# Performance work log

Measured on AMD Instinct MI355X. Metric: run time of the kernel, lower is better.

## Reference

```python
import jax, jax.numpy as jnp
import numpy as np

D_MODEL = 512
NUM_HEADS = 8
D_K = D_MODEL // NUM_HEADS


def setup_inputs() -> dict:
    key = jax.random.key(0)
    ks = jax.random.split(key, 11)
    B, S = 2, 4096
    std = max(0.02, min((1.0 / D_MODEL) ** 0.5, 0.5))
    xavier = (6.0 / (D_MODEL + D_MODEL)) ** 0.5
    return {
        "Q": jax.random.normal(ks[0], (B, S, D_MODEL), jnp.float32),
        "K": jax.random.normal(ks[1], (B, S, D_MODEL), jnp.float32),
        "V": jax.random.normal(ks[2], (B, S, D_MODEL), jnp.float32),
        # torch Linear convention: weight [out, in], y = x @ W.T + b
        "Wq": std * jax.random.truncated_normal(ks[3], -2.0, 2.0, (D_MODEL, D_MODEL), jnp.float32),
        "bq": jnp.zeros((D_MODEL,), jnp.float32),
        "Wk": std * jax.random.truncated_normal(ks[4], -2.0, 2.0, (D_MODEL, D_MODEL), jnp.float32),
        "bk": jnp.zeros((D_MODEL,), jnp.float32),
        "Wv": std * jax.random.truncated_normal(ks[5], -2.0, 2.0, (D_MODEL, D_MODEL), jnp.float32),
        "bv": jnp.zeros((D_MODEL,), jnp.float32),
        "Wo": jax.random.uniform(ks[6], (D_MODEL, D_MODEL), jnp.float32, -xavier, xavier),
        "bo": jnp.zeros((D_MODEL,), jnp.float32),
    }


def _split_heads(x):
    B, S, _ = x.shape
    return x.reshape(B, S, NUM_HEADS, D_K).transpose(0, 2, 1, 3)  # [B,H,S,dk]


def reference(Q, K, V, Wq, bq, Wk, bk, Wv, bv, Wo, bo):
    B, S, _ = Q.shape
    q = _split_heads(Q @ Wq.T + bq)
    k = _split_heads(K @ Wk.T + bk)
    v = _split_heads(V @ Wv.T + bv)
    scores = jnp.einsum("bhqd,bhkd->bhqk", q, k) / (D_K ** 0.5)  # [B,H,S,S]
    causal = jnp.tril(jnp.ones((S, S), bool))  # mask=True path
    scores = jnp.where(causal[None, None], scores, jnp.float32(-1e9))
    attn = jax.nn.softmax(scores, axis=-1)
    out = jnp.einsum("bhqk,bhkd->bhqd", attn, v)
    out = out.transpose(0, 2, 1, 3).reshape(B, S, D_MODEL)
    return out @ Wo.T + bo, attn
```

## Files before the change

kernel.cpp:

```cpp
#include <hip/hip_runtime.h>
#include <stdint.h>

#define B_  2
#define H_  8
#define S_  4096
#define DM_ 512
#define DK_ 64
#define BH_ (B_*H_)

using f32x4 = __attribute__((ext_vector_type(4))) float;
using s16x8 = __attribute__((ext_vector_type(8))) short;
using u16x4 = __attribute__((ext_vector_type(4))) unsigned short;

__device__ __forceinline__ unsigned short f2bf(float f) {
    unsigned int u = __float_as_uint(f);
    u += 0x7FFFu + ((u >> 16) & 1u);
    return (unsigned short)(u >> 16);
}
__device__ __forceinline__ float bf2f(unsigned short h) {
    return __uint_as_float(((unsigned int)h) << 16);
}

template<int MODE>
__global__ __launch_bounds__(256) void proj_kernel(
        const float* __restrict__ X, const float* __restrict__ W,
        const float* __restrict__ bias, unsigned short* __restrict__ Y,
        float scale)
{
    __shared__ __align__(16) unsigned short xh[64*40], xl[64*40];
    __shared__ __align__(16) unsigned short wh[64*40], wl[64*40];
    const int tid  = threadIdx.x;
    const int wave = tid >> 6, lane = tid & 63, lq = lane >> 4, lr = lane & 15;
    const int m0 = blockIdx.x * 64, n0 = blockIdx.y * 64;

    f32x4 acc[4] = {{0.f,0.f,0.f,0.f},{0.f,0.f,0.f,0.f},
                    {0.f,0.f,0.f,0.f},{0.f,0.f,0.f,0.f}};

    for (int kk = 0; kk < 16; ++kk) {
        __syncthreads();
#pragma unroll
        for (int p = 0; p < 2; ++p) {
            int idx = tid + p*256;
            int row = idx >> 3, seg = idx & 7;
            float4 xv = *(const float4*)&X[(size_t)(m0+row)*DM_ + kk*32 + seg*4];
            float4 wv = *(const float4*)&W[(size_t)(n0+row)*DM_ + kk*32 + seg*4];
            float xs4[4] = {xv.x, xv.y, xv.z, xv.w};
            float ws4[4] = {wv.x, wv.y, wv.z, wv.w};
            u16x4 xhi, xlo, whi, wlo;
#pragma unroll
            for (int i = 0; i < 4; ++i) {
                unsigned short h = f2bf(xs4[i]); xhi[i] = h; xlo[i] = f2bf(xs4[i] - bf2f(h));
                unsigned short g = f2bf(ws4[i]); whi[i] = g; wlo[i] = f2bf(ws4[i] - bf2f(g));
            }
            *(u16x4*)&xh[row*40 + seg*4] = xhi;
            *(u16x4*)&xl[row*40 + seg*4] = xlo;
            *(u16x4*)&wh[row*40 + seg*4] = whi;
            *(u16x4*)&wl[row*40 + seg*4] = wlo;
        }
        __syncthreads();
        const int ar = wave*16 + lr;
        s16x8 ah = *(const s16x8*)&xh[ar*40 + lq*8];
        s16x8 al = *(const s16x8*)&xl[ar*40 + lq*8];
#pragma unroll
        for (int nt = 0; nt < 4; ++nt) {
            int br = nt*16 + lr;
            s16x8 bh8 = *(const s16x8*)&wh[br*40 + lq*8];
            s16x8 bl8 = *(const s16x8*)&wl[br*40 + lq*8];
            acc[nt] = __builtin_amdgcn_mfma_f32_16x16x32_bf16(ah, bh8, acc[nt], 0, 0, 0);
            acc[nt] = __builtin_amdgcn_mfma_f32_16x16x32_bf16(ah, bl8, acc[nt], 0, 0, 0);
            acc[nt] = __builtin_amdgcn_mfma_f32_16x16x32_bf16(al, bh8, acc[nt], 0, 0, 0);
        }
    }
#pragma unroll
    for (int nt = 0; nt < 4; ++nt)
#pragma unroll
        for (int r = 0; r < 4; ++r) {
            int m = m0 + wave*16 + lq*4 + r;
            int n = n0 + nt*16 + lr;
            float v = (acc[nt][r] + bias[n]) * scale;
            int b = m >> 12, s = m & 4095;
            int h = n >> 6,  d = n & 63;
            size_t addr;
            if (MODE == 0) addr = ((size_t)((b*H_ + h)*S_ + s))*DK_ + d;
            else           addr = ((size_t)((b*H_ + h)*DK_ + d))*S_ + s;
            Y[addr] = f2bf(v);
        }
}

__global__ __launch_bounds__(256) void stats_kernel(
        const unsigned short* __restrict__ qb, const unsigned short* __restrict__ kb,
        float* __restrict__ lsum)
{
    __shared__ __align__(16) unsigned short qs[64*72], ks[32*72];
    const int tid  = threadIdx.x;
    const int wave = tid >> 6, lane = tid & 63, lq = lane >> 4, lr = lane & 15;
    const int bh = blockIdx.y;
    const int s0 = blockIdx.x * 64;

#pragma unroll
    for (int p = 0; p < 2; ++p) {
        int idx = tid + p*256;
        int row = idx >> 3, seg = idx & 7;
        *(s16x8*)&qs[row*72 + seg*8] =
            *(const s16x8*)&qb[((size_t)bh*S_ + s0 + row)*DK_ + seg*8];
    }
    __syncthreads();
    const int ar = wave*16 + lr;
    s16x8 aq0 = *(const s16x8*)&qs[ar*72 +  0 + lq*8];
    s16x8 aq1 = *(const s16x8*)&qs[ar*72 + 32 + lq*8];

    float lacc[4] = {0.f, 0.f, 0.f, 0.f};
    const int jtmax = (s0 + 63) >> 5;
    for (int jt = 0; jt <= jtmax; ++jt) {
        __syncthreads();
        {
            int row = tid >> 3, seg = tid & 7;
            *(s16x8*)&ks[row*72 + seg*8] =
                *(const s16x8*)&kb[((size_t)bh*S_ + jt*32 + row)*DK_ + seg*8];
        }
        __syncthreads();
#pragma unroll
        for (int nt = 0; nt < 2; ++nt) {
            int br = nt*16 + lr;
            s16x8 b0 = *(const s16x8*)&ks[br*72 +  0 + lq*8];
            s16x8 b1 = *(const s16x8*)&ks[br*72 + 32 + lq*8];
            f32x4 sc = {0.f,0.f,0.f,0.f};
            sc = __builtin_amdgcn_mfma_f32_16x16x32_bf16(aq0, b0, sc, 0, 0, 0);
            sc = __builtin_amdgcn_mfma_f32_16x16x32_bf16(aq1, b1, sc, 0, 0, 0);
            int j = jt*32 + nt*16 + lr;
#pragma unroll
            for (int r = 0; r < 4; ++r) {
                int sq = s0 + wave*16 + lq*4 + r;
                lacc[r] += (j <= sq) ? __expf(sc[r] - 16.f) : 0.f;
            }
        }
    }
#pragma unroll
    for (int r = 0; r < 4; ++r) {
        float v = lacc[r];
        for (int off = 1; off < 16; off <<= 1) v += __shfl_xor(v, off, 64);
        if (lr == 0) lsum[(size_t)bh*S_ + s0 + wave*16 + lq*4 + r] = v;
    }
}

__global__ __launch_bounds__(256) void attn_kernel(
        const unsigned short* __restrict__ qb, const unsigned short* __restrict__ kb,
        const unsigned short* __restrict__ vtb, const float* __restrict__ lsum,
        float* __restrict__ attn, unsigned short* __restrict__ oacc)
{
    __shared__ __align__(16) unsigned short qs[64*72], ks[32*72], vs[64*40];
    __shared__ __align__(16) unsigned short ps[4][16*40];
    __shared__ float invl[64];
    const int tid  = threadIdx.x;
    const int wave = tid >> 6, lane = tid & 63, lq = lane >> 4, lr = lane & 15;
    const int bh = blockIdx.y;
    const int s0 = blockIdx.x * 64;

#pragma unroll
    for (int p = 0; p < 2; ++p) {
        int idx = tid + p*256;
        int row = idx >> 3, seg = idx & 7;
        *(s16x8*)&qs[row*72 + seg*8] =
            *(const s16x8*)&qb[((size_t)bh*S_ + s0 + row)*DK_ + seg*8];
    }
    if (tid < 64) invl[tid] = 1.0f / lsum[(size_t)bh*S_ + s0 + tid];
    __syncthreads();
    const int ar = wave*16 + lr;
    s16x8 aq0 = *(const s16x8*)&qs[ar*72 +  0 + lq*8];
    s16x8 aq1 = *(const s16x8*)&qs[ar*72 + 32 + lq*8];
    float il[4];
#pragma unroll
    for (int r = 0; r < 4; ++r) il[r] = invl[wave*16 + lq*4 + r];

    f32x4 O[4] = {{0.f,0.f,0.f,0.f},{0.f,0.f,0.f,0.f},
                  {0.f,0.f,0.f,0.f},{0.f,0.f,0.f,0.f}};
    const int jtcomp = (s0 + 63) >> 5;

    for (int jt = 0; jt < S_/32; ++jt) {
        if (jt <= jtcomp) {
            __syncthreads();
            {
                int row = tid >> 3, seg = tid & 7;
                *(s16x8*)&ks[row*72 + seg*8] =
                    *(const s16x8*)&kb[((size_t)bh*S_ + jt*32 + row)*DK_ + seg*8];
            }
            {
                int d = tid >> 2, seg = tid & 3;
                *(s16x8*)&vs[d*40 + seg*8] =
                    *(const s16x8*)&vtb[((size_t)bh*DK_ + d)*S_ + jt*32 + seg*8];
            }
            __syncthreads();
#pragma unroll
            for (int nt = 0; nt < 2; ++nt) {
                int br = nt*16 + lr;
                s16x8 b0 = *(const s16x8*)&ks[br*72 +  0 + lq*8];
                s16x8 b1 = *(const s16x8*)&ks[br*72 + 32 + lq*8];
                f32x4 sc = {0.f,0.f,0.f,0.f};
                sc = __builtin_amdgcn_mfma_f32_16x16x32_bf16(aq0, b0, sc, 0, 0, 0);
                sc = __builtin_amdgcn_mfma_f32_16x16x32_bf16(aq1, b1, sc, 0, 0, 0);
                int j = jt*32 + nt*16 + lr;
#pragma unroll
                for (int r = 0; r < 4; ++r) {
                    int sq = s0 + wave*16 + lq*4 + r;
                    float p = (j <= sq) ? __expf(sc[r] - 16.f) : 0.f;
                    float a = p * il[r];
                    attn[((size_t)bh*S_ + sq)*S_ + j] = a;
                    ps[wave][(lq*4 + r)*40 + nt*16 + lr] = f2bf(a);
                }
            }
            __syncthreads();
            s16x8 ap = *(const s16x8*)&ps[wave][lr*40 + lq*8];
#pragma unroll
            for (int nt = 0; nt < 4; ++nt) {
                s16x8 bv = *(const s16x8*)&vs[(nt*16 + lr)*40 + lq*8];
                O[nt] = __builtin_amdgcn_mfma_f32_16x16x32_bf16(ap, bv, O[nt], 0, 0, 0);
            }
        } else {
#pragma unroll
            for (int p = 0; p < 2; ++p) {
                int idx = tid + p*256;
                int row = idx >> 3, c4 = idx & 7;
                float4 z = {0.f, 0.f, 0.f, 0.f};
                *(float4*)&attn[((size_t)bh*S_ + s0 + row)*S_ + jt*32 + c4*4] = z;
            }
        }
    }
    const int b = bh >> 3, h = bh & 7;
#pragma unroll
    for (int nt = 0; nt < 4; ++nt)
#pragma unroll
        for (int r = 0; r < 4; ++r) {
            int s = s0 + wave*16 + lq*4 + r;
            oacc[((size_t)(b*S_ + s))*DM_ + h*DK_ + nt*16 + lr] = f2bf(O[nt][r]);
        }
}

__global__ __launch_bounds__(256) void outproj_kernel(
        const unsigned short* __restrict__ Xin, const float* __restrict__ W,
        const float* __restrict__ bias, float* __restrict__ out)
{
    __shared__ __align__(16) unsigned short xs[64*40], wh[64*40];
    const int tid  = threadIdx.x;
    const int wave = tid >> 6, lane = tid & 63, lq = lane >> 4, lr = lane & 15;
    const int m0 = blockIdx.x * 64, n0 = blockIdx.y * 64;

    f32x4 acc[4] = {{0.f,0.f,0.f,0.f},{0.f,0.f,0.f,0.f},
                    {0.f,0.f,0.f,0.f},{0.f,0.f,0.f,0.f}};

    for (int kk = 0; kk < 16; ++kk) {
        __syncthreads();
        {
            int row = tid >> 2, seg = tid & 3;
            *(s16x8*)&xs[row*40 + seg*8] =
                *(const s16x8*)&Xin[(size_t)(m0+row)*DM_ + kk*32 + seg*8];
        }
#pragma unroll
        for (int p = 0; p < 2; ++p) {
            int idx = tid + p*256;
            int row = idx >> 3, seg = idx & 7;
            float4 wv = *(const float4*)&W[(size_t)(n0+row)*DM_ + kk*32 + seg*4];
            u16x4 whi;
            whi[0] = f2bf(wv.x); whi[1] = f2bf(wv.y);
            whi[2] = f2bf(wv.z); whi[3] = f2bf(wv.w);
            *(u16x4*)&wh[row*40 + seg*4] = whi;
        }
        __syncthreads();
        s16x8 a = *(const s16x8*)&xs[(wave*16 + lr)*40 + lq*8];
#pragma unroll
        for (int nt = 0; nt < 4; ++nt) {
            s16x8 b = *(const s16x8*)&wh[(nt*16 + lr)*40 + lq*8];
            acc[nt] = __builtin_amdgcn_mfma_f32_16x16x32_bf16(a, b, acc[nt], 0, 0, 0);
        }
    }
#pragma unroll
    for (int nt = 0; nt < 4; ++nt)
#pragma unroll
        for (int r = 0; r < 4; ++r) {
            int m = m0 + wave*16 + lq*4 + r;
            int n = n0 + nt*16 + lr;
            out[(size_t)m*DM_ + n] = acc[nt][r] + bias[n];
        }
}

extern "C" void kernel_launch(void* const* d_in, const int* in_sizes, int n_in,
                              void* d_out, int out_size, void* d_ws, size_t ws_size,
                              hipStream_t stream)
{
    const float* Q  = (const float*)d_in[0];
    const float* K  = (const float*)d_in[1];
    const float* V  = (const float*)d_in[2];
    const float* Wq = (const float*)d_in[3];  const float* bq = (const float*)d_in[4];
    const float* Wk = (const float*)d_in[5];  const float* bk = (const float*)d_in[6];
    const float* Wv = (const float*)d_in[7];  const float* bv = (const float*)d_in[8];
    const float* Wo = (const float*)d_in[9];  const float* bo = (const float*)d_in[10];

    char* ws = (char*)d_ws;
    const size_t QKV_BYTES = (size_t)BH_ * S_ * DK_ * sizeof(unsigned short);
    unsigned short* qbf  = (unsigned short*)(ws);
    unsigned short* kbf  = (unsigned short*)(ws + QKV_BYTES);
    unsigned short* vtb  = (unsigned short*)(ws + 2*QKV_BYTES);
    float*          lsum = (float*)(ws + 3*QKV_BYTES);
    unsigned short* oacc = (unsigned short*)(ws + 3*QKV_BYTES + (size_t)BH_*S_*sizeof(float));

    float* out0 = (float*)d_out;
    float* attn = out0 + (size_t)B_ * S_ * DM_;

    dim3 blk(256);
    proj_kernel<0><<<dim3(128, 8), blk, 0, stream>>>(Q, Wq, bq, qbf, 0.125f);
    proj_kernel<0><<<dim3(128, 8), blk, 0, stream>>>(K, Wk, bk, kbf, 1.0f);
    proj_kernel<1><<<dim3(128, 8), blk, 0, stream>>>(V, Wv, bv, vtb, 1.0f);
    stats_kernel  <<<dim3(64, 16), blk, 0, stream>>>(qbf, kbf, lsum);
    attn_kernel   <<<dim3(64, 16), blk, 0, stream>>>(qbf, kbf, vtb, lsum, attn, oacc);
    outproj_kernel<<<dim3(128, 8), blk, 0, stream>>>(oacc, Wo, bo, out0);
}
```

Baseline: 1.497 ms.

## Pre-split inputs to bf16 hi/lo, widen K tiles to 64 across kernels

Adds separate conversion kernels that split the inputs and weights into bf16 hi/lo arrays once, so the projection GEMMs no longer redo the split for every output tile. The GEMMs, stats and attention kernels now use 64-wide K/key tiles, which halves loop iterations and barriers. The attention kernel also replaces a block barrier with a per-wave LDS wait and groups the attention-matrix stores after the PV MFMAs. The cost is extra launches and extra global traffic for the converted copies, plus larger shared-memory use.

```diff
diff --git a/kernel.cpp b/kernel.cpp
--- a/kernel.cpp
+++ b/kernel.cpp
@@ -11,6 +11,7 @@
 using f32x4 = __attribute__((ext_vector_type(4))) float;
 using s16x8 = __attribute__((ext_vector_type(8))) short;
 using u16x4 = __attribute__((ext_vector_type(4))) unsigned short;
+using u16x8 = __attribute__((ext_vector_type(8))) unsigned short;
 
 __device__ __forceinline__ unsigned short f2bf(float f) {
     unsigned int u = __float_as_uint(f);
@@ -21,14 +22,42 @@
     return __uint_as_float(((unsigned int)h) << 16);
 }
 
+__global__ __launch_bounds__(256) void convert_split(const float* __restrict__ in,
+        unsigned short* __restrict__ hi, unsigned short* __restrict__ lo, int n4)
+{
+    for (int i = blockIdx.x*256 + threadIdx.x; i < n4; i += gridDim.x*256) {
+        float4 v = ((const float4*)in)[i];
+        float s4[4] = {v.x, v.y, v.z, v.w};
+        u16x4 h, l;
+#pragma unroll
+        for (int j = 0; j < 4; ++j) {
+            unsigned short hh = f2bf(s4[j]);
+            h[j] = hh; l[j] = f2bf(s4[j] - bf2f(hh));
+        }
+        ((u16x4*)hi)[i] = h;
+        ((u16x4*)lo)[i] = l;
+    }
+}
+
+__global__ __launch_bounds__(256) void convert_hi(const float* __restrict__ in,
+        unsigned short* __restrict__ hi, int n4)
+{
+    for (int i = blockIdx.x*256 + threadIdx.x; i < n4; i += gridDim.x*256) {
+        float4 v = ((const float4*)in)[i];
+        u16x4 h;
+        h[0] = f2bf(v.x); h[1] = f2bf(v.y); h[2] = f2bf(v.z); h[3] = f2bf(v.w);
+        ((u16x4*)hi)[i] = h;
+    }
+}
+
 template<int MODE>
 __global__ __launch_bounds__(256) void proj_kernel(
-        const float* __restrict__ X, const float* __restrict__ W,
-        const float* __restrict__ bias, unsigned short* __restrict__ Y,
-        float scale)
-{
-    __shared__ __align__(16) unsigned short xh[64*40], xl[64*40];
-    __shared__ __align__(16) unsigned short wh[64*40], wl[64*40];
+        const unsigned short* __restrict__ Xh, const unsigned short* __restrict__ Xl,
+        const unsigned short* __restrict__ Wh, const unsigned short* __restrict__ Wl,
+        const float* __restrict__ bias, unsigned short* __restrict__ Y, float scale)
+{
+    __shared__ __align__(16) unsigned short xh[64*72], xl[64*72];
+    __shared__ __align__(16) unsigned short wh[64*72], wl[64*72];
     const int tid  = threadIdx.x;
     const int wave = tid >> 6, lane = tid & 63, lq = lane >> 4, lr = lane & 15;
     const int m0 = blockIdx.x * 64, n0 = blockIdx.y * 64;
@@ -36,39 +65,38 @@
     f32x4 acc[4] = {{0.f,0.f,0.f,0.f},{0.f,0.f,0.f,0.f},
                     {0.f,0.f,0.f,0.f},{0.f,0.f,0.f,0.f}};
 
-    for (int kk = 0; kk < 16; ++kk) {
+    for (int kk = 0; kk < 8; ++kk) {
         __syncthreads();
 #pragma unroll
         for (int p = 0; p < 2; ++p) {
             int idx = tid + p*256;
             int row = idx >> 3, seg = idx & 7;
-            float4 xv = *(const float4*)&X[(size_t)(m0+row)*DM_ + kk*32 + seg*4];
-            float4 wv = *(const float4*)&W[(size_t)(n0+row)*DM_ + kk*32 + seg*4];
-            float xs4[4] = {xv.x, xv.y, xv.z, xv.w};
-            float ws4[4] = {wv.x, wv.y, wv.z, wv.w};
-            u16x4 xhi, xlo, whi, wlo;
-#pragma unroll
-            for (int i = 0; i < 4; ++i) {
-                unsigned short h = f2bf(xs4[i]); xhi[i] = h; xlo[i] = f2bf(xs4[i] - bf2f(h));
-                unsigned short g = f2bf(ws4[i]); whi[i] = g; wlo[i] = f2bf(ws4[i] - bf2f(g));
-            }
-            *(u16x4*)&xh[row*40 + seg*4] = xhi;
-            *(u16x4*)&xl[row*40 + seg*4] = xlo;
-            *(u16x4*)&wh[row*40 + seg*4] = whi;
-            *(u16x4*)&wl[row*40 + seg*4] = wlo;
+            size_t xoff = (size_t)(m0+row)*DM_ + kk*64 + seg*8;
+            size_t woff = (size_t)(n0+row)*DM_ + kk*64 + seg*8;
+            *(u16x8*)&xh[row*72 + seg*8] = *(const u16x8*)&Xh[xoff];
+            *(u16x8*)&xl[row*72 + seg*8] = *(const u16x8*)&Xl[xoff];
+            *(u16x8*)&wh[row*72 + seg*8] = *(const u16x8*)&Wh[woff];
+            *(u16x8*)&wl[row*72 + seg*8] = *(const u16x8*)&Wl[woff];
         }
         __syncthreads();
         const int ar = wave*16 + lr;
-        s16x8 ah = *(const s16x8*)&xh[ar*40 + lq*8];
-        s16x8 al = *(const s16x8*)&xl[ar*40 + lq*8];
+        s16x8 ah0 = *(const s16x8*)&xh[ar*72 +  0 + lq*8];
+        s16x8 ah1 = *(const s16x8*)&xh[ar*72 + 32 + lq*8];
+        s16x8 al0 = *(const s16x8*)&xl[ar*72 +  0 + lq*8];
+        s16x8 al1 = *(const s16x8*)&xl[ar*72 + 32 + lq*8];
 #pragma unroll
         for (int nt = 0; nt < 4; ++nt) {
             int br = nt*16 + lr;
-            s16x8 bh8 = *(const s16x8*)&wh[br*40 + lq*8];
-            s16x8 bl8 = *(const s16x8*)&wl[br*40 + lq*8];
-            acc[nt] = __builtin_amdgcn_mfma_f32_16x16x32_bf16(ah, bh8, acc[nt], 0, 0, 0);
-            acc[nt] = __builtin_amdgcn_mfma_f32_16x16x32_bf16(ah, bl8, acc[nt], 0, 0, 0);
-            acc[nt] = __builtin_amdgcn_mfma_f32_16x16x32_bf16(al, bh8, acc[nt], 0, 0, 0);
+            s16x8 bh0 = *(const s16x8*)&wh[br*72 +  0 + lq*8];
+            s16x8 bh1 = *(const s16x8*)&wh[br*72 + 32 + lq*8];
+            s16x8 bl0 = *(const s16x8*)&wl[br*72 +  0 + lq*8];
+            s16x8 bl1 = *(const s16x8*)&wl[br*72 + 32 + lq*8];
+            acc[nt] = __builtin_amdgcn_mfma_f32_16x16x32_bf16(ah0, bh0, acc[nt], 0, 0, 0);
+            acc[nt] = __builtin_amdgcn_mfma_f32_16x16x32_bf16(ah0, bl0, acc[nt], 0, 0, 0);
+            acc[nt] = __builtin_amdgcn_mfma_f32_16x16x32_bf16(al0, bh0, acc[nt], 0, 0, 0);
+            acc[nt] = __builtin_amdgcn_mfma_f32_16x16x32_bf16(ah1, bh1, acc[nt], 0, 0, 0);
+            acc[nt] = __builtin_amdgcn_mfma_f32_16x16x32_bf16(ah1, bl1, acc[nt], 0, 0, 0);
+            acc[nt] = __builtin_amdgcn_mfma_f32_16x16x32_bf16(al1, bh1, acc[nt], 0, 0, 0);
         }
     }
 #pragma unroll
@@ -91,7 +119,7 @@
         const unsigned short* __restrict__ qb, const unsigned short* __restrict__ kb,
         float* __restrict__ lsum)
 {
-    __shared__ __align__(16) unsigned short qs[64*72], ks[32*72];
+    __shared__ __align__(16) unsigned short qs[64*72], ks[64*72];
     const int tid  = threadIdx.x;
     const int wave = tid >> 6, lane = tid & 63, lq = lane >> 4, lr = lane & 15;
     const int bh = blockIdx.y;
@@ -110,24 +138,26 @@
     s16x8 aq1 = *(const s16x8*)&qs[ar*72 + 32 + lq*8];
 
     float lacc[4] = {0.f, 0.f, 0.f, 0.f};
-    const int jtmax = (s0 + 63) >> 5;
+    const int jtmax = blockIdx.x;
     for (int jt = 0; jt <= jtmax; ++jt) {
         __syncthreads();
-        {
-            int row = tid >> 3, seg = tid & 7;
+#pragma unroll
+        for (int p = 0; p < 2; ++p) {
+            int idx = tid + p*256;
+            int row = idx >> 3, seg = idx & 7;
             *(s16x8*)&ks[row*72 + seg*8] =
-                *(const s16x8*)&kb[((size_t)bh*S_ + jt*32 + row)*DK_ + seg*8];
-        }
-        __syncthreads();
-#pragma unroll
-        for (int nt = 0; nt < 2; ++nt) {
+                *(const s16x8*)&kb[((size_t)bh*S_ + jt*64 + row)*DK_ + seg*8];
+        }
+        __syncthreads();
+#pragma unroll
+        for (int nt = 0; nt < 4; ++nt) {
             int br = nt*16 + lr;
             s16x8 b0 = *(const s16x8*)&ks[br*72 +  0 + lq*8];
             s16x8 b1 = *(const s16x8*)&ks[br*72 + 32 + lq*8];
             f32x4 sc = {0.f,0.f,0.f,0.f};
             sc = __builtin_amdgcn_mfma_f32_16x16x32_bf16(aq0, b0, sc, 0, 0, 0);
             sc = __builtin_amdgcn_mfma_f32_16x16x32_bf16(aq1, b1, sc, 0, 0, 0);
-            int j = jt*32 + nt*16 + lr;
+            int j = jt*64 + nt*16 + lr;
 #pragma unroll
             for (int r = 0; r < 4; ++r) {
                 int sq = s0 + wave*16 + lq*4 + r;
@@ -148,8 +178,8 @@
         const unsigned short* __restrict__ vtb, const float* __restrict__ lsum,
         float* __restrict__ attn, unsigned short* __restrict__ oacc)
 {
-    __shared__ __align__(16) unsigned short qs[64*72], ks[32*72], vs[64*40];
-    __shared__ __align__(16) unsigned short ps[4][16*40];
+    __shared__ __align__(16) unsigned short qs[64*72], ks[64*72], vs[64*72];
+    __shared__ __align__(16) unsigned short ps[4][16*72];
     __shared__ float invl[64];
     const int tid  = threadIdx.x;
     const int wave = tid >> 6, lane = tid & 63, lq = lane >> 4, lr = lane & 15;
@@ -174,54 +204,65 @@
 
     f32x4 O[4] = {{0.f,0.f,0.f,0.f},{0.f,0.f,0.f,0.f},
                   {0.f,0.f,0.f,0.f},{0.f,0.f,0.f,0.f}};
-    const int jtcomp = (s0 + 63) >> 5;
-
-    for (int jt = 0; jt < S_/32; ++jt) {
+    const int jtcomp = blockIdx.x;
+
+    for (int jt = 0; jt < S_/64; ++jt) {
         if (jt <= jtcomp) {
             __syncthreads();
-            {
-                int row = tid >> 3, seg = tid & 7;
+#pragma unroll
+            for (int p = 0; p < 2; ++p) {
+                int idx = tid + p*256;
+                int row = idx >> 3, seg = idx & 7;
                 *(s16x8*)&ks[row*72 + seg*8] =
-                    *(const s16x8*)&kb[((size_t)bh*S_ + jt*32 + row)*DK_ + seg*8];
-            }
-            {
-                int d = tid >> 2, seg = tid & 3;
-                *(s16x8*)&vs[d*40 + seg*8] =
-                    *(const s16x8*)&vtb[((size_t)bh*DK_ + d)*S_ + jt*32 + seg*8];
+                    *(const s16x8*)&kb[((size_t)bh*S_ + jt*64 + row)*DK_ + seg*8];
+                *(s16x8*)&vs[row*72 + seg*8] =
+                    *(const s16x8*)&vtb[((size_t)bh*DK_ + row)*S_ + jt*64 + seg*8];
             }
             __syncthreads();
-#pragma unroll
-            for (int nt = 0; nt < 2; ++nt) {
+            float a_all[4][4];
+#pragma unroll
+            for (int nt = 0; nt < 4; ++nt) {
                 int br = nt*16 + lr;
                 s16x8 b0 = *(const s16x8*)&ks[br*72 +  0 + lq*8];
                 s16x8 b1 = *(const s16x8*)&ks[br*72 + 32 + lq*8];
                 f32x4 sc = {0.f,0.f,0.f,0.f};
                 sc = __builtin_amdgcn_mfma_f32_16x16x32_bf16(aq0, b0, sc, 0, 0, 0);
                 sc = __builtin_amdgcn_mfma_f32_16x16x32_bf16(aq1, b1, sc, 0, 0, 0);
-                int j = jt*32 + nt*16 + lr;
+                int j = jt*64 + nt*16 + lr;
 #pragma unroll
                 for (int r = 0; r < 4; ++r) {
                     int sq = s0 + wave*16 + lq*4 + r;
                     float p = (j <= sq) ? __expf(sc[r] - 16.f) : 0.f;
                     float a = p * il[r];
-                    attn[((size_t)bh*S_ + sq)*S_ + j] = a;
-                    ps[wave][(lq*4 + r)*40 + nt*16 + lr] = f2bf(a);
+                    a_all[nt][r] = a;
+                    ps[wave][(lq*4 + r)*72 + nt*16 + lr] = f2bf(a);
                 }
             }
-            __syncthreads();
-            s16x8 ap = *(const s16x8*)&ps[wave][lr*40 + lq*8];
+            asm volatile("s_waitcnt lgkmcnt(0)" ::: "memory");
+            __builtin_amdgcn_sched_barrier(0);
+            s16x8 ap0 = *(const s16x8*)&ps[wave][lr*72 +  0 + lq*8];
+            s16x8 ap1 = *(const s16x8*)&ps[wave][lr*72 + 32 + lq*8];
 #pragma unroll
             for (int nt = 0; nt < 4; ++nt) {
-                s16x8 bv = *(const s16x8*)&vs[(nt*16 + lr)*40 + lq*8];
-                O[nt] = __builtin_amdgcn_mfma_f32_16x16x32_bf16(ap, bv, O[nt], 0, 0, 0);
-            }
+                s16x8 bv0 = *(const s16x8*)&vs[(nt*16 + lr)*72 +  0 + lq*8];
+                s16x8 bv1 = *(const s16x8*)&vs[(nt*16 + lr)*72 + 32 + lq*8];
+                O[nt] = __builtin_amdgcn_mfma_f32_16x16x32_bf16(ap0, bv0, O[nt], 0, 0, 0);
+                O[nt] = __builtin_amdgcn_mfma_f32_16x16x32_bf16(ap1, bv1, O[nt], 0, 0, 0);
+            }
+#pragma unroll
+            for (int nt = 0; nt < 4; ++nt)
+#pragma unroll
+                for (int r = 0; r < 4; ++r) {
+                    int sq = s0 + wave*16 + lq*4 + r;
+                    attn[((size_t)bh*S_ + sq)*S_ + jt*64 + nt*16 + lr] = a_all[nt][r];
+                }
         } else {
 #pragma unroll
-            for (int p = 0; p < 2; ++p) {
+            for (int p = 0; p < 4; ++p) {
                 int idx = tid + p*256;
-                int row = idx >> 3, c4 = idx & 7;
+                int row = idx >> 4, c4 = idx & 15;
                 float4 z = {0.f, 0.f, 0.f, 0.f};
-                *(float4*)&attn[((size_t)bh*S_ + s0 + row)*S_ + jt*32 + c4*4] = z;
+                *(float4*)&attn[((size_t)bh*S_ + s0 + row)*S_ + jt*64 + c4*4] = z;
             }
         }
     }
@@ -236,10 +277,10 @@
 }
 
 __global__ __launch_bounds__(256) void outproj_kernel(
-        const unsigned short* __restrict__ Xin, const float* __restrict__ W,
+        const unsigned short* __restrict__ Xin, const unsigned short* __restrict__ Woh,
         const float* __restrict__ bias, float* __restrict__ out)
 {
-    __shared__ __align__(16) unsigned short xs[64*40], wh[64*40];
+    __shared__ __align__(16) unsigned short xs[64*72], wsm[64*72];
     const int tid  = threadIdx.x;
     const int wave = tid >> 6, lane = tid & 63, lq = lane >> 4, lr = lane & 15;
     const int m0 = blockIdx.x * 64, n0 = blockIdx.y * 64;
@@ -247,29 +288,28 @@
     f32x4 acc[4] = {{0.f,0.f,0.f,0.f},{0.f,0.f,0.f,0.f},
                     {0.f,0.f,0.f,0.f},{0.f,0.f,0.f,0.f}};
 
-    for (int kk = 0; kk < 16; ++kk) {
-        __syncthreads();
-        {
-            int row = tid >> 2, seg = tid & 3;
-            *(s16x8*)&xs[row*40 + seg*8] =
-                *(const s16x8*)&Xin[(size_t)(m0+row)*DM_ + kk*32 + seg*8];
-        }
+    for (int kk = 0; kk < 8; ++kk) {
+        __syncthreads();
 #pragma unroll
         for (int p = 0; p < 2; ++p) {
             int idx = tid + p*256;
             int row = idx >> 3, seg = idx & 7;
-            float4 wv = *(const float4*)&W[(size_t)(n0+row)*DM_ + kk*32 + seg*4];
-            u16x4 whi;
-            whi[0] = f2bf(wv.x); whi[1] = f2bf(wv.y);
-            whi[2] = f2bf(wv.z); whi[3] = f2bf(wv.w);
-            *(u16x4*)&wh[row*40 + seg*4] = whi;
-        }
-        __syncthreads();
-        s16x8 a = *(const s16x8*)&xs[(wave*16 + lr)*40 + lq*8];
+            *(s16x8*)&xs [row*72 + seg*8] =
+                *(const s16x8*)&Xin[(size_t)(m0+row)*DM_ + kk*64 + seg*8];
+            *(s16x8*)&wsm[row*72 + seg*8] =
+                *(const s16x8*)&Woh[(size_t)(n0+row)*DM_ + kk*64 + seg*8];
+        }
+        __syncthreads();
+        const int ar = wave*16 + lr;
+        s16x8 a0 = *(const s16x8*)&xs[ar*72 +  0 + lq*8];
+        s16x8 a1 = *(const s16x8*)&xs[ar*72 + 32 + lq*8];
 #pragma unroll
         for (int nt = 0; nt < 4; ++nt) {
-            s16x8 b = *(const s16x8*)&wh[(nt*16 + lr)*40 + lq*8];
-            acc[nt] = __builtin_amdgcn_mfma_f32_16x16x32_bf16(a, b, acc[nt], 0, 0, 0);
+            int br = nt*16 + lr;
+            s16x8 b0 = *(const s16x8*)&wsm[br*72 +  0 + lq*8];
+            s16x8 b1 = *(const s16x8*)&wsm[br*72 + 32 + lq*8];
+            acc[nt] = __builtin_amdgcn_mfma_f32_16x16x32_bf16(a0, b0, acc[nt], 0, 0, 0);
+            acc[nt] = __builtin_amdgcn_mfma_f32_16x16x32_bf16(a1, b1, acc[nt], 0, 0, 0);
         }
     }
 #pragma unroll
@@ -296,20 +336,44 @@
 
     char* ws = (char*)d_ws;
     const size_t QKV_BYTES = (size_t)BH_ * S_ * DK_ * sizeof(unsigned short);
+    const size_t W_BYTES   = (size_t)DM_ * DM_ * sizeof(unsigned short);
     unsigned short* qbf  = (unsigned short*)(ws);
     unsigned short* kbf  = (unsigned short*)(ws + QKV_BYTES);
     unsigned short* vtb  = (unsigned short*)(ws + 2*QKV_BYTES);
     float*          lsum = (float*)(ws + 3*QKV_BYTES);
     unsigned short* oacc = (unsigned short*)(ws + 3*QKV_BYTES + (size_t)BH_*S_*sizeof(float));
+    char* p = ws + 4*QKV_BYTES + (size_t)BH_*S_*sizeof(float);
+    unsigned short* xh  = (unsigned short*)(p);               p += QKV_BYTES;
+    unsigned short* xl  = (unsigned short*)(p);               p += QKV_BYTES;
+    unsigned short* wqh = (unsigned short*)(p);               p += W_BYTES;
+    unsigned short* wql = (unsigned short*)(p);               p += W_BYTES;
+    unsigned short* wkh = (unsigned short*)(p);               p += W_BYTES;
+    unsigned short* wkl = (unsigned short*)(p);               p += W_BYTES;
+    unsigned short* wvh = (unsigned short*)(p);               p += W_BYTES;
+    unsigned short* wvl = (unsigned short*)(p);               p += W_BYTES;
+    unsigned short* woh = (unsigned short*)(p);               p += W_BYTES;
 
     float* out0 = (float*)d_out;
     float* attn = out0 + (size_t)B_ * S_ * DM_;
 
     dim3 blk(256);
-    proj_kernel<0><<<dim3(128, 8), blk, 0, stream>>>(Q, Wq, bq, qbf, 0.125f);
-    proj_kernel<0><<<dim3(128, 8), blk, 0, stream>>>(K, Wk, bk, kbf, 1.0f);
-    proj_kernel<1><<<dim3(128, 8), blk, 0, stream>>>(V, Wv, bv, vtb, 1.0f);
+    const int n4x = B_*S_*DM_/4;
+    const int n4w = DM_*DM_/4;
+    auto cgrid = [](int n4) { int g = (n4 + 255) / 256; return g > 2048 ? 2048 : g; };
+
+    convert_split<<<cgrid(n4w), blk, 0, stream>>>(Wq, wqh, wql, n4w);
+    convert_split<<<cgrid(n4w), blk, 0, stream>>>(Wk, wkh, wkl, n4w);
+    convert_split<<<cgrid(n4w), blk, 0, stream>>>(Wv, wvh, wvl, n4w);
+    convert_hi   <<<cgrid(n4w), blk, 0, stream>>>(Wo, woh, n4w);
+
+    convert_split<<<cgrid(n4x), blk, 0, stream>>>(Q, xh, xl, n4x);
+    proj_kernel<0><<<dim3(128, 8), blk, 0, stream>>>(xh, xl, wqh, wql, bq, qbf, 0.125f);
+    convert_split<<<cgrid(n4x), blk, 0, stream>>>(K, xh, xl, n4x);
+    proj_kernel<0><<<dim3(128, 8), blk, 0, stream>>>(xh, xl, wkh, wkl, bk, kbf, 1.0f);
+    convert_split<<<cgrid(n4x), blk, 0, stream>>>(V, xh, xl, n4x);
+    proj_kernel<1><<<dim3(128, 8), blk, 0, stream>>>(xh, xl, wvh, wvl, bv, vtb, 1.0f);
+
     stats_kernel  <<<dim3(64, 16), blk, 0, stream>>>(qbf, kbf, lsum);
     attn_kernel   <<<dim3(64, 16), blk, 0, stream>>>(qbf, kbf, vtb, lsum, attn, oacc);
-    outproj_kernel<<<dim3(128, 8), blk, 0, stream>>>(oacc, Wo, bo, out0);
-}
+    outproj_kernel<<<dim3(128, 8), blk, 0, stream>>>(oacc, woh, bo, out0);
+}
```

Result: faster. 1.387 ms (-7.4%).
